# Kernel tuning notes

Hardware: AMD Instinct MI355X
Metric: run time of the kernel (lower is better)

Reference implementation:

```python
import jax, jax.numpy as jnp
import numpy as np

HID = 256        # constant.hidden_size
EMB = 256        # constant.embedding_size
STATE_NUM = 5    # constant.state_num
PAD_ID = 0


def _lstm(x, Wih, Whh, b):
    # x: (N, T, D) -> (N, T, H); single-layer unidirectional, PyTorch gate order i,f,g,o
    N = x.shape[0]
    Hh = Whh.shape[1]
    def step(carry, xt):
        h, c = carry
        g = xt @ Wih.T + h @ Whh.T + b
        i, f, gg, o = jnp.split(g, 4, axis=-1)
        c = jax.nn.sigmoid(f) * c + jax.nn.sigmoid(i) * jnp.tanh(gg)
        h = jax.nn.sigmoid(o) * jnp.tanh(c)
        return (h, c), h
    h0 = jnp.zeros((N, Hh), x.dtype)
    _, ys = jax.lax.scan(step, (h0, h0), jnp.swapaxes(x, 0, 1))
    return jnp.swapaxes(ys, 0, 1)


def setup_inputs() -> dict:
    rng = np.random.RandomState(0)
    B, L, W, V = 8, 128, 48, 50000
    S = STATE_NUM
    P = L // (S - 1)
    batch_utterances = jnp.asarray(rng.randint(0, V, size=(B, L, W)), jnp.int32)
    utterance_sequence_length = jnp.asarray(rng.randint(1, W + 1, size=(B, L)), jnp.int32)
    perm = np.stack([b * L + rng.permutation(L) for b in range(B)]).reshape(-1)
    session_transpose_matrix = jnp.asarray(perm, jnp.int32)
    stm = np.zeros((B, L, S), np.int32)  # col 0 == 0 -> new-state slot (projection path)
    carry = rng.rand(B, L, S - 1) < 0.3
    pos = rng.randint(1, P + 1, size=(B, L, S - 1))
    stm[:, :, 1:] = np.where(carry, -1, pos)
    state_transition_matrix = jnp.asarray(stm)

    def w(*shape):
        return jnp.asarray(rng.randn(*shape) * 0.05, jnp.float32)

    return dict(
        batch_utterances=batch_utterances,
        utterance_sequence_length=utterance_sequence_length,
        session_transpose_matrix=session_transpose_matrix,
        state_transition_matrix=state_transition_matrix,
        max_conversation_length=L,
        emb=w(V, EMB),
        utt_Wih=w(4 * HID, EMB), utt_Whh=w(4 * HID, HID), utt_b=w(4 * HID),
        ws1=w(HID, HID), ws2=w(1, HID),
        conv_Wih=w(4 * HID, HID), conv_Whh=w(4 * HID, HID), conv_b=w(4 * HID),
        sess_Wih=w(4 * HID, HID), sess_Whh=w(4 * HID, HID), sess_b=w(4 * HID),
        Wp=w(HID, 2 * HID), bp=w(HID),
        Ws=w(HID, 2 * HID), bs=w(HID),
    )


def reference(batch_utterances, utterance_sequence_length, session_transpose_matrix,
              state_transition_matrix, max_conversation_length,
              emb, utt_Wih, utt_Whh, utt_b, ws1, ws2,
              conv_Wih, conv_Whh, conv_b, sess_Wih, sess_Whh, sess_b,
              Wp, bp, Ws, bs):
    B, L, W = batch_utterances.shape
    S = STATE_NUM
    P = L // (S - 1)
    Lc = int(max_conversation_length)

    # --- UtteranceEncoder: embedding lookup + word-level LSTM ---
    tok = batch_utterances.reshape(-1, W)            # (B*L, W)
    word_out = _lstm(emb[tok], utt_Wih, utt_Whh, utt_b)  # (B*L, W, H)

    # --- SelfAttentiveEncoder (1 hop) ---
    hbar = jnp.tanh(word_out @ ws1.T)                # (B*L, W, H)
    logits = (hbar @ ws2.T)[..., 0]                  # (B*L, W)
    logits = logits + (-10000.0) * (tok == PAD_ID).astype(logits.dtype)
    alphas = jax.nn.softmax(logits, axis=1)
    att = jnp.einsum('nw,nwh->nh', alphas, word_out).reshape(B, L, HID)

    # --- ConversationEncoder ---
    conv = _lstm(att, conv_Wih, conv_Whh, conv_b)    # (B, L, H)

    # --- SessionEncoder: gather-permute utterances into sessions, LSTM per session ---
    flat = att.reshape(-1, HID)[session_transpose_matrix]       # (B*L, H)
    sess_in = flat.reshape(B * (S - 1), P, HID)
    sess_out = _lstm(sess_in, sess_Wih, sess_Whh, sess_b).reshape(B, S - 1, P, HID)

    # --- StateMatrixEncoder: sequential scatter/gather scan over conversation steps ---
    sess_idx = jnp.clip(jnp.arange(S) - 1, 0, S - 2)            # (S,)
    gathered = sess_out[:, sess_idx]                            # (B, S, P, H)
    conv_shift = jnp.concatenate([conv[:, :1], conv[:, :L - 1]], axis=1)  # conv_repre[i-1] (i==0 -> [0])
    stm_T = jnp.swapaxes(state_transition_matrix, 0, 1)         # (L, B, S)
    cs_T = jnp.swapaxes(conv_shift, 0, 1)                       # (L, B, H)

    def step(prev_row, inp):
        stm_i, cs = inp                                         # (B,S), (B,H)
        posn = jnp.clip(stm_i - 1, 0, P - 1)
        v_g = jnp.take_along_axis(gathered, posn[:, :, None, None], axis=2)[:, :, 0, :]  # (B,S,H)
        is_carry = (stm_i == -1)[..., None]
        is_gather = (stm_i > 0)[..., None]
        v = jnp.where(is_carry, prev_row, jnp.where(is_gather, v_g, 0.0))
        # AvgPool2d((S-1,1)) over exactly S-1 collected vectors == masked mean
        one_res = jnp.sum(jnp.where(stm_i[..., None] != 0, v, 0.0), axis=1) / (S - 1)
        new0 = jax.nn.relu(jnp.concatenate([one_res, cs], axis=-1) @ Wp.T + bp)
        row = jnp.where(is_gather, v_g, 0.0).at[:, 0, :].set(new0)
        return row, row

    _, rows = jax.lax.scan(step, jnp.zeros((B, S, HID), att.dtype), (stm_T, cs_T))
    state_matrix = jnp.swapaxes(rows, 0, 1)                     # (B, L, S, H)

    # --- ScoresCalculator (unidirectional -> LogSoftmax) ---
    uc = jnp.concatenate([att[:, :Lc], conv[:, :Lc]], axis=-1)  # (B, Lc, 2H)
    up = jax.nn.relu(uc @ Ws.T + bs)                            # (B, Lc, H)
    scores = jnp.einsum('blsh,blh->bls', state_matrix[:, :Lc], up)
    return jax.nn.log_softmax(scores, axis=2)
```

## Files before the change

### kernel.cpp

```cpp
#include <hip/hip_runtime.h>
#include <hip/hip_bf16.h>
#include <math.h>

#define HIDN 256
#define GATES 1024
#define BB 8
#define LLEN 128
#define WLEN 48
#define SNUM 5
#define PLEN 32
#define NSEQ 1024
#define EMBD 256

typedef _Float16 f16;
typedef _Float16 h2_t __attribute__((ext_vector_type(2)));
typedef short short8_t __attribute__((ext_vector_type(8)));
typedef float f32x4 __attribute__((ext_vector_type(4)));

__device__ __forceinline__ float sigf(float x){ return 1.0f/(1.0f+expf(-x)); }

__device__ __forceinline__ unsigned short f2bf(float f){
  unsigned int x = __builtin_bit_cast(unsigned int, f);
  x += 0x7fffu + ((x >> 16) & 1u);
  return (unsigned short)(x >> 16);
}
__device__ __forceinline__ float bf2f(unsigned short u){
  unsigned int x = ((unsigned int)u) << 16;
  return __builtin_bit_cast(float, x);
}

__device__ __forceinline__ float fd2(unsigned int w, unsigned int h, float acc){
  h2_t wa = __builtin_bit_cast(h2_t, w);
  h2_t hb = __builtin_bit_cast(h2_t, h);
#if defined(__has_builtin)
#if __has_builtin(__builtin_amdgcn_fdot2)
  return __builtin_amdgcn_fdot2(wa, hb, acc, false);
#else
  return acc + (float)wa[0]*(float)hb[0] + (float)wa[1]*(float)hb[1];
#endif
#else
  return acc + (float)wa[0]*(float)hb[0] + (float)wa[1]*(float)hb[1];
#endif
}

__device__ __forceinline__ float dot8(uint4 w, uint4 h, float acc){
  acc = fd2(w.x, h.x, acc);
  acc = fd2(w.y, h.y, acc);
  acc = fd2(w.z, h.z, acc);
  acc = fd2(w.w, h.w, acc);
  return acc;
}

template<bool GATHER, bool BIAS, bool RELU, bool SPLIT>
__global__ __launch_bounds__(256) void gemm_abt64_k(
  const float* __restrict__ A, const float* __restrict__ A2,
  const float* __restrict__ Bm, const float* __restrict__ bias,
  float* __restrict__ C, const int* __restrict__ gidx,
  int K, int N, int ostride)
{
  __shared__ float As[32][68];
  __shared__ float Bs[32][68];
  const int tid = threadIdx.x;
  const int m0 = blockIdx.x*64, n0 = blockIdx.y*64;
  const int tx = tid & 15, ty = tid >> 4;
  const int lr = tid >> 3;
  const int lc = (tid & 7) * 4;
  float acc[4][4] = {};
  for (int k0 = 0; k0 < K; k0 += 32){
    #pragma unroll
    for (int hf = 0; hf < 2; ++hf){
      const int r = lr + hf*32;
      int am = m0 + r;
      if (GATHER) am = gidx[am];
      const float* asrc;
      if (SPLIT){
        if (k0 < 256) asrc = A  + (size_t)am*256 + k0 + lc;
        else          asrc = A2 + (size_t)am*256 + (k0-256) + lc;
      } else {
        asrc = A + (size_t)am*K + k0 + lc;
      }
      float4 av = *reinterpret_cast<const float4*>(asrc);
      float4 bv = *reinterpret_cast<const float4*>(Bm + (size_t)(n0+r)*K + k0 + lc);
      As[lc+0][r]=av.x; As[lc+1][r]=av.y; As[lc+2][r]=av.z; As[lc+3][r]=av.w;
      Bs[lc+0][r]=bv.x; Bs[lc+1][r]=bv.y; Bs[lc+2][r]=bv.z; Bs[lc+3][r]=bv.w;
    }
    __syncthreads();
    #pragma unroll
    for (int kk = 0; kk < 32; ++kk){
      const float4 a = *reinterpret_cast<const float4*>(&As[kk][ty*4]);
      const float4 b = *reinterpret_cast<const float4*>(&Bs[kk][tx*4]);
      acc[0][0] += a.x*b.x; acc[0][1] += a.x*b.y; acc[0][2] += a.x*b.z; acc[0][3] += a.x*b.w;
      acc[1][0] += a.y*b.x; acc[1][1] += a.y*b.y; acc[1][2] += a.y*b.z; acc[1][3] += a.y*b.w;
      acc[2][0] += a.z*b.x; acc[2][1] += a.z*b.y; acc[2][2] += a.z*b.z; acc[2][3] += a.z*b.w;
      acc[3][0] += a.w*b.x; acc[3][1] += a.w*b.y; acc[3][2] += a.w*b.z; acc[3][3] += a.w*b.w;
    }
    __syncthreads();
  }
  float4 bb;
  if (BIAS) bb = *reinterpret_cast<const float4*>(bias + n0 + tx*4);
  else      { bb.x=0.f; bb.y=0.f; bb.z=0.f; bb.w=0.f; }
  #pragma unroll
  for (int i = 0; i < 4; ++i){
    float4 o;
    o.x = acc[i][0]+bb.x; o.y = acc[i][1]+bb.y; o.z = acc[i][2]+bb.z; o.w = acc[i][3]+bb.w;
    if (RELU){ o.x=fmaxf(o.x,0.f); o.y=fmaxf(o.y,0.f); o.z=fmaxf(o.z,0.f); o.w=fmaxf(o.w,0.f); }
    *reinterpret_cast<float4*>(C + (size_t)(m0+ty*4+i)*ostride + n0 + tx*4) = o;
  }
}

__global__ __launch_bounds__(256) void cvt_w16_k(
  const float* __restrict__ a, const float* __restrict__ b,
  f16* __restrict__ oa, f16* __restrict__ ob)
{
  const int i = blockIdx.x*256 + threadIdx.x;
  oa[i] = (f16)a[i];
  ob[i] = (f16)b[i];
}

__global__ __launch_bounds__(256) void cvt_bf16_k(
  const float* __restrict__ a, unsigned short* __restrict__ o, int n)
{
  for (int i = blockIdx.x*256 + threadIdx.x; i < n; i += gridDim.x*256)
    o[i] = f2bf(a[i]);
}

__global__ __launch_bounds__(256) void remap_k(const int* __restrict__ tok, int* __restrict__ gidx2){
  const int idx = blockIdx.x*256 + threadIdx.x;
  const int t = idx >> 10, u = idx & 1023;
  gidx2[idx] = tok[u*WLEN + t];
}

__global__ __launch_bounds__(256) void xgemm_k(
  const float* __restrict__ emb, const unsigned short* __restrict__ Wb,
  const float* __restrict__ bias, const int* __restrict__ gidx,
  float* __restrict__ X)
{
  __shared__ char As[32768];
  const int tid = threadIdx.x;
  const int w = tid >> 6, l = tid & 63;
  const int lr = l & 15, lg = l >> 4;
  const int m0 = blockIdx.x*64, n0 = blockIdx.y*64;
  #pragma unroll
  for (int rr = 0; rr < 4; ++rr){
    const int rl = rr*16 + (tid >> 4);
    const int c4 = tid & 15;
    const float* src = emb + (size_t)gidx[m0 + rl]*256;
    const int sw = (rl & 7) << 4;
    #pragma unroll
    for (int q = 0; q < 4; ++q){
      const int idx4 = c4 + q*16;
      float4 v = reinterpret_cast<const float4*>(src)[idx4];
      union { unsigned long long u; unsigned short us[4]; } pk;
      pk.us[0]=f2bf(v.x); pk.us[1]=f2bf(v.y); pk.us[2]=f2bf(v.z); pk.us[3]=f2bf(v.w);
      *reinterpret_cast<unsigned long long*>(As + rl*512 + ((idx4*8) ^ sw)) = pk.u;
    }
  }
  __syncthreads();
  short8_t a[8];
  #pragma unroll
  for (int ks = 0; ks < 8; ++ks){
    const int rl = w*16 + lr;
    a[ks] = *reinterpret_cast<const short8_t*>(As + rl*512 + ((ks*64 + lg*16) ^ ((rl&7)<<4)));
  }
  #pragma unroll
  for (int nt = 0; nt < 4; ++nt){
    f32x4 acc = f32x4{0,0,0,0};
    const int n = n0 + nt*16 + lr;
    #pragma unroll
    for (int ks = 0; ks < 8; ++ks){
      short8_t b = *reinterpret_cast<const short8_t*>(Wb + (size_t)n*256 + ks*32 + lg*8);
      acc = __builtin_amdgcn_mfma_f32_16x16x32_bf16(a[ks], b, acc, 0, 0, 0);
    }
    const float bn = bias[n];
    #pragma unroll
    for (int r = 0; r < 4; ++r){
      const int m = m0 + w*16 + lg*4 + r;
      X[(size_t)m*1024 + n] = acc[r] + bn;
    }
  }
}

__global__ __launch_bounds__(256, 1) void word_stream_k(
  const float* __restrict__ X, const unsigned short* __restrict__ Wb,
  unsigned short* __restrict__ woutb)
{
  extern __shared__ char smem[];
  const int tid = threadIdx.x;
  const int w = tid >> 6, l = tid & 63;
  const int lr = l & 15, lg = l >> 4;
  const int S0 = blockIdx.x * 16;
  char* wlds = smem + w*32768;
  char* hb0 = smem + 131072;
  char* hb1 = smem + 139264;

  #pragma unroll
  for (int rr = 0; rr < 16; ++rr){
    const int rl = rr*4 + lg;
    const unsigned short* src = Wb + (size_t)(768 + w*64 + rl)*256;
    const int sw = (rl & 7) << 4;
    short8_t v0 = *reinterpret_cast<const short8_t*>(src + lr*8);
    short8_t v1 = *reinterpret_cast<const short8_t*>(src + (lr+16)*8);
    *reinterpret_cast<short8_t*>(wlds + rl*512 + ((lr*16) ^ sw)) = v0;
    *reinterpret_cast<short8_t*>(wlds + rl*512 + (((lr+16)*16) ^ sw)) = v1;
  }
  short8_t wr[96];
  #pragma unroll
  for (int g = 0; g < 3; ++g){
    #pragma unroll
    for (int jt = 0; jt < 4; ++jt){
      #pragma unroll
      for (int ks = 0; ks < 8; ++ks){
        const int n = g*256 + w*64 + jt*16 + lr;
        wr[(g*4 + jt)*8 + ks] = *reinterpret_cast<const short8_t*>(
            Wb + (size_t)n*256 + ks*32 + lg*8);
      }
    }
  }
  float c_reg[4][4] = {};
  __syncthreads();

  for (int t = 0; t < WLEN; ++t){
    const char* hr = (t & 1) ? hb1 : hb0;
    char* hw = (t & 1) ? hb0 : hb1;
    #pragma unroll
    for (int jt = 0; jt < 4; ++jt){
      f32x4 acc0 = f32x4{0,0,0,0}, acc1 = f32x4{0,0,0,0};
      f32x4 acc2 = f32x4{0,0,0,0}, acc3 = f32x4{0,0,0,0};
      #pragma unroll
      for (int ks = 0; ks < 8; ++ks){
        short8_t a;
        if (t == 0){
          a = short8_t{0,0,0,0,0,0,0,0};
        } else {
          const int kb = ks*64 + lg*16;
          a = *reinterpret_cast<const short8_t*>(hr + lr*512 + (kb ^ ((lr & 7) << 4)));
        }
        acc0 = __builtin_amdgcn_mfma_f32_16x16x32_bf16(a, wr[(0*4+jt)*8+ks], acc0, 0, 0, 0);
        acc1 = __builtin_amdgcn_mfma_f32_16x16x32_bf16(a, wr[(1*4+jt)*8+ks], acc1, 0, 0, 0);
        acc2 = __builtin_amdgcn_mfma_f32_16x16x32_bf16(a, wr[(2*4+jt)*8+ks], acc2, 0, 0, 0);
        const int rl_o = jt*16 + lr;
        short8_t bo = *reinterpret_cast<const short8_t*>(
            wlds + rl_o*512 + ((ks*64 + lg*16) ^ ((rl_o & 7) << 4)));
        acc3 = __builtin_amdgcn_mfma_f32_16x16x32_bf16(a, bo, acc3, 0, 0, 0);
      }
      const int j = w*64 + jt*16 + lr;
      #pragma unroll
      for (int r = 0; r < 4; ++r){
        const int s = lg*4 + r;
        const float* xp = X + ((size_t)t*1024 + (S0+s))*1024 + j;
        float gi = acc0[r] + xp[0];
        float gf = acc1[r] + xp[256];
        float gg = acc2[r] + xp[512];
        float go = acc3[r] + xp[768];
        float cc = sigf(gf)*c_reg[jt][r] + sigf(gi)*tanhf(gg);
        c_reg[jt][r] = cc;
        float hh = sigf(go)*tanhf(cc);
        unsigned short hb16 = f2bf(hh);
        woutb[((size_t)(S0+s)*WLEN + t)*256 + j] = hb16;
        *reinterpret_cast<unsigned short*>(hw + s*512 + ((j*2) ^ ((s & 7) << 4))) = hb16;
      }
    }
    __syncthreads();
  }
}

__global__ __launch_bounds__(256) void attlog_k(
  const unsigned short* __restrict__ woutb, const unsigned short* __restrict__ ws1b,
  const float* __restrict__ ws2, float* __restrict__ logits)
{
  const int tid = threadIdx.x;
  const int w = tid >> 6, l = tid & 63;
  const int lr = l & 15, lg = l >> 4;
  const int m0 = blockIdx.x*64;
  short8_t a[8];
  #pragma unroll
  for (int ks = 0; ks < 8; ++ks){
    const int m = m0 + w*16 + lr;
    a[ks] = *reinterpret_cast<const short8_t*>(woutb + (size_t)m*256 + ks*32 + lg*8);
  }
  float part[4] = {0.f, 0.f, 0.f, 0.f};
  #pragma unroll
  for (int nt = 0; nt < 16; ++nt){
    f32x4 acc = f32x4{0,0,0,0};
    const int n = nt*16 + lr;
    #pragma unroll
    for (int ks = 0; ks < 8; ++ks){
      short8_t b = *reinterpret_cast<const short8_t*>(ws1b + (size_t)n*256 + ks*32 + lg*8);
      acc = __builtin_amdgcn_mfma_f32_16x16x32_bf16(a[ks], b, acc, 0, 0, 0);
    }
    const float w2 = ws2[n];
    #pragma unroll
    for (int r = 0; r < 4; ++r) part[r] += w2 * tanhf(acc[r]);
  }
  #pragma unroll
  for (int r = 0; r < 4; ++r){
    float p = part[r];
    p += __shfl_xor(p, 1, 64);
    p += __shfl_xor(p, 2, 64);
    p += __shfl_xor(p, 4, 64);
    p += __shfl_xor(p, 8, 64);
    if (lr == 0) logits[m0 + w*16 + lg*4 + r] = p;
  }
}

__global__ __launch_bounds__(256) void att_softmax_k(
  const unsigned short* __restrict__ woutb, const float* __restrict__ logits,
  const int* __restrict__ tok, float* __restrict__ att)
{
  __shared__ float e[WLEN];
  __shared__ float den_s;
  const int n = blockIdx.x, j = threadIdx.x;
  if (j < WLEN){
    float lgt = logits[n*WLEN + j];
    if (tok[n*WLEN + j] == 0) lgt -= 10000.0f;
    e[j] = lgt;
  }
  __syncthreads();
  if (j == 0){
    float mx = -1e30f;
    for (int ww = 0; ww < WLEN; ++ww) mx = fmaxf(mx, e[ww]);
    float den = 0.f;
    for (int ww = 0; ww < WLEN; ++ww){ float ee = expf(e[ww]-mx); e[ww] = ee; den += ee; }
    den_s = den;
  }
  __syncthreads();
  const float inv = 1.0f/den_s;
  float a = 0.f;
  for (int ww = 0; ww < WLEN; ++ww)
    a += e[ww]*bf2f(woutb[((size_t)n*WLEN + ww)*HIDN + j]);
  att[(size_t)n*HIDN + j] = a*inv;
}

__global__ __launch_bounds__(256) void word_gates_k(
    const int* __restrict__ tok, const float* __restrict__ emb,
    const float* __restrict__ Wih, const float* __restrict__ Whh,
    const float* __restrict__ bias, const float* __restrict__ hbuf,
    float* __restrict__ G, int t)
{
  __shared__ float As[32][68];
  __shared__ float Bs[32][68];
  const int tid = threadIdx.x;
  const int m0 = blockIdx.x*64, n0 = blockIdx.y*64;
  const int tx = tid & 15, ty = tid >> 4;
  const int lr = tid >> 3;
  const int lc = (tid & 7) * 4;
  float acc[4][4] = {};
  for (int kt = 0; kt < 16; ++kt){
    const int k0 = (kt & 7)*32;
    const bool xp = (kt < 8);
    #pragma unroll
    for (int hf = 0; hf < 2; ++hf){
      const int r = lr + hf*32;
      float4 av, bv;
      if (xp){
        const int token = tok[(m0+r)*WLEN + t];
        av = *reinterpret_cast<const float4*>(emb + (size_t)token*EMBD + k0 + lc);
      } else {
        av = *reinterpret_cast<const float4*>(hbuf + (size_t)(m0+r)*HIDN + k0 + lc);
      }
      const float* bptr = (xp ? Wih : Whh) + (size_t)(n0+r)*HIDN + k0 + lc;
      bv = *reinterpret_cast<const float4*>(bptr);
      As[lc+0][r]=av.x; As[lc+1][r]=av.y; As[lc+2][r]=av.z; As[lc+3][r]=av.w;
      Bs[lc+0][r]=bv.x; Bs[lc+1][r]=bv.y; Bs[lc+2][r]=bv.z; Bs[lc+3][r]=bv.w;
    }
    __syncthreads();
    #pragma unroll
    for (int kk = 0; kk < 32; ++kk){
      const float4 a = *reinterpret_cast<const float4*>(&As[kk][ty*4]);
      const float4 b = *reinterpret_cast<const float4*>(&Bs[kk][tx*4]);
      acc[0][0] += a.x*b.x; acc[0][1] += a.x*b.y; acc[0][2] += a.x*b.z; acc[0][3] += a.x*b.w;
      acc[1][0] += a.y*b.x; acc[1][1] += a.y*b.y; acc[1][2] += a.y*b.z; acc[1][3] += a.y*b.w;
      acc[2][0] += a.z*b.x; acc[2][1] += a.z*b.y; acc[2][2] += a.z*b.z; acc[2][3] += a.z*b.w;
      acc[3][0] += a.w*b.x; acc[3][1] += a.w*b.y; acc[3][2] += a.w*b.z; acc[3][3] += a.w*b.w;
    }
    __syncthreads();
  }
  const float4 bb = *reinterpret_cast<const float4*>(bias + n0 + tx*4);
  #pragma unroll
  for (int i = 0; i < 4; ++i){
    float4 o;
    o.x = acc[i][0]+bb.x; o.y = acc[i][1]+bb.y; o.z = acc[i][2]+bb.z; o.w = acc[i][3]+bb.w;
    *reinterpret_cast<float4*>(G + (size_t)(m0+ty*4+i)*GATES + n0 + tx*4) = o;
  }
}

__global__ __launch_bounds__(256) void word_update_k(
  const float* __restrict__ G, float* __restrict__ h, float* __restrict__ c,
  unsigned short* __restrict__ woutb, int t)
{
  int idx = blockIdx.x*256 + threadIdx.x;
  int m = idx >> 8, j = idx & 255;
  const float* g = G + (size_t)m*GATES;
  float gi = g[j], gf = g[HIDN+j], gg = g[2*HIDN+j], go = g[3*HIDN+j];
  float cc = c[idx];
  cc = sigf(gf)*cc + sigf(gi)*tanhf(gg);
  float hh = sigf(go)*tanhf(cc);
  c[idx] = cc; h[idx] = hh;
  woutb[(size_t)m*WLEN*HIDN + (size_t)t*HIDN + j] = f2bf(hh);
}

__global__ __launch_bounds__(512, 2) void recur512_k(
  const float* __restrict__ xwc, const f16* __restrict__ w16c, float* __restrict__ convb,
  const float* __restrict__ xws, const f16* __restrict__ w16s, float* __restrict__ soutb)
{
  const float* xw; const f16* w16; float* out; int seq, T;
  if (blockIdx.x < 8){ seq = blockIdx.x;     T = 128; xw = xwc; w16 = w16c; out = convb; }
  else               { seq = blockIdx.x - 8; T = 32;  xw = xws; w16 = w16s; out = soutb; }

  extern __shared__ char smem[];
  uint4* w_lds  = (uint4*)smem;
  float* g_s    = (float*)(smem + 131072);
  f16*   h_half = (f16*)(smem + 131072 + 4096);
  const uint4* h4 = (const uint4*)h_half;

  const int tid = threadIdx.x;
  const int n0 = tid, n1 = tid + 512;

  #pragma unroll
  for (int cth = 0; cth < 8; ++cth){
    w_lds[cth*1024 + n0] = *reinterpret_cast<const uint4*>(w16 + (size_t)n0*HIDN + 192 + cth*8);
    w_lds[cth*1024 + n1] = *reinterpret_cast<const uint4*>(w16 + (size_t)n1*HIDN + 192 + cth*8);
  }
  uint4 wr0[24], wr1[24];
  #pragma unroll
  for (int cth = 0; cth < 24; ++cth){
    wr0[cth] = *reinterpret_cast<const uint4*>(w16 + (size_t)n0*HIDN + cth*8);
    wr1[cth] = *reinterpret_cast<const uint4*>(w16 + (size_t)n1*HIDN + cth*8);
  }
  if (tid < 128) reinterpret_cast<uint4*>(h_half)[tid >> 2] = uint4{0,0,0,0};
  float c_reg = 0.f;
  __syncthreads();

  for (int t = 0; t < T; ++t){
    float acc0 = xw[(size_t)(seq*T + t)*GATES + n0];
    float acc1 = xw[(size_t)(seq*T + t)*GATES + n1];
    float a0=0.f, a1=0.f, a2=0.f, a3=0.f;
    #pragma unroll
    for (int k = 0; k < 24; k += 4){
      const uint4 h0 = h4[k+0], h1 = h4[k+1], h2 = h4[k+2], h3 = h4[k+3];
      a0 = dot8(wr0[k+0], h0, a0);
      a1 = dot8(wr0[k+1], h1, a1);
      a2 = dot8(wr0[k+2], h2, a2);
      a3 = dot8(wr0[k+3], h3, a3);
      acc1 = dot8(wr1[k+0], h0, acc1);
      acc1 = dot8(wr1[k+1], h1, acc1);
      acc1 = dot8(wr1[k+2], h2, acc1);
      acc1 = dot8(wr1[k+3], h3, acc1);
    }
    #pragma unroll
    for (int cth = 0; cth < 8; ++cth){
      const uint4 hv = h4[24 + cth];
      const uint4 w0 = w_lds[cth*1024 + n0];
      const uint4 w1 = w_lds[cth*1024 + n1];
      a0 = dot8(w0, hv, a0);
      acc1 = dot8(w1, hv, acc1);
    }
    g_s[n0] = acc0 + (a0+a1) + (a2+a3);
    g_s[n1] = acc1;
    __syncthreads();
    if (tid < HIDN){
      const int j = tid;
      float gi = g_s[j], gf = g_s[HIDN+j], gg = g_s[2*HIDN+j], go = g_s[3*HIDN+j];
      float cc = sigf(gf)*c_reg + sigf(gi)*tanhf(gg);
      c_reg = cc;
      float hh = sigf(go)*tanhf(cc);
      h_half[j] = (f16)hh;
      out[(size_t)(seq*T + t)*HIDN + j] = hh;
    }
    __syncthreads();
  }
}

__global__ __launch_bounds__(256) void scan_prep_k(
  const float* __restrict__ sess_out, const float* __restrict__ conv_out,
  const int* __restrict__ stm, float* __restrict__ state, float* __restrict__ onec)
{
  const int bl = blockIdx.x;
  const int b = bl >> 7, l = bl & 127;
  const int j = threadIdx.x;
  float ones = 0.f;
  #pragma unroll
  for (int s = 1; s < SNUM; ++s){
    const int sv = stm[(size_t)bl*SNUM + s];
    float vg = 0.f;
    if (sv > 0){
      int p = sv - 1; if (p > PLEN-1) p = PLEN-1;
      vg = sess_out[((size_t)(b*4 + (s-1))*PLEN + p)*HIDN + j];
    }
    float v = vg;
    if (sv == -1){
      v = 0.f;
      if (l > 0){
        const int pv = stm[(size_t)(bl-1)*SNUM + s];
        if (pv > 0){
          int p2 = pv - 1; if (p2 > PLEN-1) p2 = PLEN-1;
          v = sess_out[((size_t)(b*4 + (s-1))*PLEN + p2)*HIDN + j];
        }
      }
    }
    if (sv != 0) ones += v;
    state[((size_t)bl*SNUM + s)*HIDN + j] = vg;
  }
  onec[(size_t)bl*(2*HIDN) + j] = ones * 0.25f;
  const int lp = (l == 0) ? 0 : (l-1);
  onec[(size_t)bl*(2*HIDN) + HIDN + j] = conv_out[((size_t)(b*LLEN + lp))*HIDN + j];
}

__global__ __launch_bounds__(256) void scores_k(
  const float* __restrict__ state, const float* __restrict__ up, float* __restrict__ out)
{
  const int n = blockIdx.x, j = threadIdx.x;
  __shared__ float red[SNUM][4];
  const float u = up[(size_t)n*HIDN + j];
  const int lane = j & 63, wid = j >> 6;
  #pragma unroll
  for (int s = 0; s < SNUM; ++s){
    float p = state[((size_t)n*SNUM + s)*HIDN + j]*u;
    for (int off = 32; off; off >>= 1) p += __shfl_down(p, off, 64);
    if (lane == 0) red[s][wid] = p;
  }
  __syncthreads();
  if (j == 0){
    float sc[SNUM]; float mx = -1e30f;
    #pragma unroll
    for (int s = 0; s < SNUM; ++s){
      sc[s] = red[s][0]+red[s][1]+red[s][2]+red[s][3];
      mx = fmaxf(mx, sc[s]);
    }
    float den = 0.f;
    #pragma unroll
    for (int s = 0; s < SNUM; ++s) den += expf(sc[s]-mx);
    const float ls = logf(den);
    #pragma unroll
    for (int s = 0; s < SNUM; ++s) out[(size_t)n*SNUM + s] = sc[s]-mx-ls;
  }
}

static const size_t OFF_G     = 0;
static const size_t OFF_H     = OFF_G     + 1048576;
static const size_t OFF_C     = OFF_H     + 262144;
static const size_t OFF_ATT   = OFF_C     + 262144;
static const size_t OFF_XWC   = OFF_ATT   + 262144;
static const size_t OFF_XWS   = OFF_XWC   + 1048576;
static const size_t OFF_CONV  = OFF_XWS   + 1048576;
static const size_t OFF_SOUT  = OFF_CONV  + 262144;
static const size_t OFF_STATE = OFF_SOUT  + 262144;
static const size_t OFF_ONEC  = OFF_STATE + 1310720;
static const size_t OFF_UP    = OFF_ONEC  + 524288;
static const size_t OFF_LOG   = OFF_UP    + 262144;
static const size_t OFF_GIDX2 = OFF_LOG   + 49152;
static const size_t OFF_W16C  = OFF_GIDX2 + 49152;
static const size_t OFF_W16S  = OFF_W16C  + 131072;
static const size_t OFF_UWHHB = OFF_W16S  + 131072;
static const size_t OFF_WIHB  = OFF_UWHHB + 131072;
static const size_t OFF_WS1B  = OFF_WIHB  + 131072;
static const size_t OFF_WOUTB = OFF_WS1B  + 32768;
static const size_t OFF_X     = OFF_WOUTB + 6291456;
static const size_t NEED_X_FLOATS = OFF_X + (size_t)49152*1024;

static const size_t WORD_LDS_BYTES  = 131072 + 2*8192;
static const size_t RECUR_LDS_BYTES = 131072 + 4096 + 512;

extern "C" void kernel_launch(void* const* d_in, const int* in_sizes, int n_in,
                              void* d_out, int out_size, void* d_ws, size_t ws_size,
                              hipStream_t stream)
{
  const int*   tok   = (const int*)  d_in[0];
  const int*   perm  = (const int*)  d_in[2];
  const int*   stm   = (const int*)  d_in[3];
  const float* emb   = (const float*)d_in[5];
  const float* uWih  = (const float*)d_in[6];
  const float* uWhh  = (const float*)d_in[7];
  const float* ub    = (const float*)d_in[8];
  const float* ws1   = (const float*)d_in[9];
  const float* ws2   = (const float*)d_in[10];
  const float* cWih  = (const float*)d_in[11];
  const float* cWhh  = (const float*)d_in[12];
  const float* cb    = (const float*)d_in[13];
  const float* sWih  = (const float*)d_in[14];
  const float* sWhh  = (const float*)d_in[15];
  const float* sb    = (const float*)d_in[16];
  const float* Wp    = (const float*)d_in[17];
  const float* bp    = (const float*)d_in[18];
  const float* Ws    = (const float*)d_in[19];
  const float* bs    = (const float*)d_in[20];

  float* wsf    = (float*)d_ws;
  float* G      = wsf + OFF_G;
  float* h      = wsf + OFF_H;
  float* c      = wsf + OFF_C;
  float* att    = wsf + OFF_ATT;
  float* xwc    = wsf + OFF_XWC;
  float* xws    = wsf + OFF_XWS;
  float* convb  = wsf + OFF_CONV;
  float* soutb  = wsf + OFF_SOUT;
  float* statem = wsf + OFF_STATE;
  float* onec   = wsf + OFF_ONEC;
  float* upb    = wsf + OFF_UP;
  float* logits = wsf + OFF_LOG;
  int*   gidx2  = (int*)(wsf + OFF_GIDX2);
  f16*   w16c   = (f16*)(wsf + OFF_W16C);
  f16*   w16s   = (f16*)(wsf + OFF_W16S);
  unsigned short* uwhhb = (unsigned short*)(wsf + OFF_UWHHB);
  unsigned short* wihb  = (unsigned short*)(wsf + OFF_WIHB);
  unsigned short* ws1b  = (unsigned short*)(wsf + OFF_WS1B);
  unsigned short* woutb = (unsigned short*)(wsf + OFF_WOUTB);
  float* X      = wsf + OFF_X;

  const bool useX = ws_size >= NEED_X_FLOATS*sizeof(float);

  hipFuncSetAttribute(reinterpret_cast<const void*>(word_stream_k),
                      hipFuncAttributeMaxDynamicSharedMemorySize, (int)WORD_LDS_BYTES);
  hipFuncSetAttribute(reinterpret_cast<const void*>(recur512_k),
                      hipFuncAttributeMaxDynamicSharedMemorySize, (int)RECUR_LDS_BYTES);

  cvt_w16_k<<<1024, 256, 0, stream>>>(cWhh, sWhh, w16c, w16s);
  cvt_bf16_k<<<256, 256, 0, stream>>>(uWhh, uwhhb, 262144);
  cvt_bf16_k<<<256, 256, 0, stream>>>(uWih, wihb, 262144);
  cvt_bf16_k<<<64, 256, 0, stream>>>(ws1, ws1b, 65536);

  if (useX){
    remap_k<<<192, 256, 0, stream>>>(tok, gidx2);
    xgemm_k<<<dim3(768,16), 256, 0, stream>>>(emb, wihb, ub, gidx2, X);
    word_stream_k<<<64, 256, WORD_LDS_BYTES, stream>>>(X, uwhhb, woutb);
  } else {
    hipMemsetAsync(h, 0, 2*262144*sizeof(float), stream);
    for (int t = 0; t < WLEN; ++t){
      word_gates_k<<<dim3(16,16), 256, 0, stream>>>(tok, emb, uWih, uWhh, ub, h, G, t);
      word_update_k<<<1024, 256, 0, stream>>>(G, h, c, woutb, t);
    }
  }

  attlog_k<<<768, 256, 0, stream>>>(woutb, ws1b, ws2, logits);
  att_softmax_k<<<1024, 256, 0, stream>>>(woutb, logits, tok, att);

  gemm_abt64_k<false,true,false,false><<<dim3(16,16), 256, 0, stream>>>(
    att, nullptr, cWih, cb, xwc, nullptr, 256, GATES, GATES);
  gemm_abt64_k<true,true,false,false><<<dim3(16,16), 256, 0, stream>>>(
    att, nullptr, sWih, sb, xws, perm, 256, GATES, GATES);

  recur512_k<<<40, 512, RECUR_LDS_BYTES, stream>>>(xwc, w16c, convb, xws, w16s, soutb);

  scan_prep_k<<<1024, 256, 0, stream>>>(soutb, convb, stm, statem, onec);
  gemm_abt64_k<false,true,true,false><<<dim3(16,4), 256, 0, stream>>>(
    onec, nullptr, Wp, bp, statem, nullptr, 512, HIDN, SNUM*HIDN);

  gemm_abt64_k<false,true,true,true><<<dim3(16,4), 256, 0, stream>>>(
    att, convb, Ws, bs, upb, nullptr, 512, HIDN, HIDN);
  scores_k<<<1024, 256, 0, stream>>>(statem, upb, (float*)d_out);
}
```

Baseline: 1.257 ms.

## Store word input gates as interleaved bf16 and use MFMA for conv/session projections

The word-level input projection now writes bf16 instead of fp32, with the four gates interleaved per hidden unit. The recurrent kernel therefore reads one 8-byte load per unit and moves half the X traffic. The word recurrence no longer holds most Whh weights in registers; it streams the i/f/g tiles from global memory (L2) each step and keeps only the o tile in LDS. It also zero-initialises h in LDS instead of branching on t==0. The conv and session input GEMMs now use a generic bf16 MFMA kernel on a bf16 copy of att. The conv/session recurrence runs 1024 threads with one gate row per thread. The trade-off is bf16 rounding of the gate pre-activations and per-step weight reloads from cache.

After: 1.668 ms. 32.7% more time.

```diff
diff --git a/kernel.cpp b/kernel.cpp
--- a/kernel.cpp
+++ b/kernel.cpp
@@ -4,12 +4,10 @@
 
 #define HIDN 256
 #define GATES 1024
-#define BB 8
 #define LLEN 128
 #define WLEN 48
 #define SNUM 5
 #define PLEN 32
-#define NSEQ 1024
 #define EMBD 256
 
 typedef _Float16 f16;
@@ -42,7 +40,6 @@
   return acc + (float)wa[0]*(float)hb[0] + (float)wa[1]*(float)hb[1];
 #endif
 }
-
 __device__ __forceinline__ float dot8(uint4 w, uint4 h, float acc){
   acc = fd2(w.x, h.x, acc);
   acc = fd2(w.y, h.y, acc);
@@ -108,6 +105,21 @@
   }
 }
 
+__global__ __launch_bounds__(256) void cvt2_k(
+  const float* __restrict__ a, const float* __restrict__ b,
+  unsigned short* __restrict__ oa, unsigned short* __restrict__ ob, int n)
+{
+  for (int i = blockIdx.x*256 + threadIdx.x; i < n; i += gridDim.x*256){
+    oa[i] = f2bf(a[i]);
+    ob[i] = f2bf(b[i]);
+  }
+}
+__global__ __launch_bounds__(256) void cvt1_k(
+  const float* __restrict__ a, unsigned short* __restrict__ o, int n)
+{
+  for (int i = blockIdx.x*256 + threadIdx.x; i < n; i += gridDim.x*256)
+    o[i] = f2bf(a[i]);
+}
 __global__ __launch_bounds__(256) void cvt_w16_k(
   const float* __restrict__ a, const float* __restrict__ b,
   f16* __restrict__ oa, f16* __restrict__ ob)
@@ -115,13 +127,6 @@
   const int i = blockIdx.x*256 + threadIdx.x;
   oa[i] = (f16)a[i];
   ob[i] = (f16)b[i];
-}
-
-__global__ __launch_bounds__(256) void cvt_bf16_k(
-  const float* __restrict__ a, unsigned short* __restrict__ o, int n)
-{
-  for (int i = blockIdx.x*256 + threadIdx.x; i < n; i += gridDim.x*256)
-    o[i] = f2bf(a[i]);
 }
 
 __global__ __launch_bounds__(256) void remap_k(const int* __restrict__ tok, int* __restrict__ gidx2){
@@ -130,10 +135,11 @@
   gidx2[idx] = tok[u*WLEN + t];
 }
 
-__global__ __launch_bounds__(256) void xgemm_k(
-  const float* __restrict__ emb, const unsigned short* __restrict__ Wb,
+template<int AMODE, bool OUT16, bool XPERM>
+__global__ __launch_bounds__(256) void mmabt_k(
+  const void* __restrict__ Asrc, const unsigned short* __restrict__ Wb,
   const float* __restrict__ bias, const int* __restrict__ gidx,
-  float* __restrict__ X)
+  void* __restrict__ Cout)
 {
   __shared__ char As[32768];
   const int tid = threadIdx.x;
@@ -141,18 +147,23 @@
   const int lr = l & 15, lg = l >> 4;
   const int m0 = blockIdx.x*64, n0 = blockIdx.y*64;
   #pragma unroll
-  for (int rr = 0; rr < 4; ++rr){
-    const int rl = rr*16 + (tid >> 4);
-    const int c4 = tid & 15;
-    const float* src = emb + (size_t)gidx[m0 + rl]*256;
-    const int sw = (rl & 7) << 4;
-    #pragma unroll
-    for (int q = 0; q < 4; ++q){
-      const int idx4 = c4 + q*16;
-      float4 v = reinterpret_cast<const float4*>(src)[idx4];
-      union { unsigned long long u; unsigned short us[4]; } pk;
-      pk.us[0]=f2bf(v.x); pk.us[1]=f2bf(v.y); pk.us[2]=f2bf(v.z); pk.us[3]=f2bf(v.w);
-      *reinterpret_cast<unsigned long long*>(As + rl*512 + ((idx4*8) ^ sw)) = pk.u;
+  for (int q = 0; q < 8; ++q){
+    const int ck = tid*8 + q;
+    const int rl = ck >> 5, o16 = ck & 31;
+    int row = m0 + rl;
+    if (AMODE <= 1) row = gidx[row];
+    char* dst = As + rl*512 + ((o16*16) ^ ((rl & 7) << 4));
+    if (AMODE == 0){
+      const float* src = (const float*)Asrc + (size_t)row*256 + o16*8;
+      float4 f0 = *reinterpret_cast<const float4*>(src);
+      float4 f1 = *reinterpret_cast<const float4*>(src + 4);
+      union { short8_t s; unsigned short u[8]; } pk;
+      pk.u[0]=f2bf(f0.x); pk.u[1]=f2bf(f0.y); pk.u[2]=f2bf(f0.z); pk.u[3]=f2bf(f0.w);
+      pk.u[4]=f2bf(f1.x); pk.u[5]=f2bf(f1.y); pk.u[6]=f2bf(f1.z); pk.u[7]=f2bf(f1.w);
+      *reinterpret_cast<short8_t*>(dst) = pk.s;
+    } else {
+      *reinterpret_cast<short8_t*>(dst) = *reinterpret_cast<const short8_t*>(
+          (const unsigned short*)Asrc + (size_t)row*256 + o16*8);
     }
   }
   __syncthreads();
@@ -160,7 +171,7 @@
   #pragma unroll
   for (int ks = 0; ks < 8; ++ks){
     const int rl = w*16 + lr;
-    a[ks] = *reinterpret_cast<const short8_t*>(As + rl*512 + ((ks*64 + lg*16) ^ ((rl&7)<<4)));
+    a[ks] = *reinterpret_cast<const short8_t*>(As + rl*512 + ((ks*64 + lg*16) ^ ((rl & 7) << 4)));
   }
   #pragma unroll
   for (int nt = 0; nt < 4; ++nt){
@@ -172,16 +183,19 @@
       acc = __builtin_amdgcn_mfma_f32_16x16x32_bf16(a[ks], b, acc, 0, 0, 0);
     }
     const float bn = bias[n];
+    const int nn = XPERM ? ((n & 255)*4 + (n >> 8)) : n;
     #pragma unroll
     for (int r = 0; r < 4; ++r){
       const int m = m0 + w*16 + lg*4 + r;
-      X[(size_t)m*1024 + n] = acc[r] + bn;
-    }
-  }
-}
-
-__global__ __launch_bounds__(256, 1) void word_stream_k(
-  const float* __restrict__ X, const unsigned short* __restrict__ Wb,
+      if (OUT16) ((unsigned short*)Cout)[(size_t)m*1024 + nn] = f2bf(acc[r] + bn);
+      else       ((float*)Cout)[(size_t)m*1024 + nn] = acc[r] + bn;
+    }
+  }
+}
+
+__global__ __launch_bounds__(256, 1) void word3_k(
+  const unsigned short* __restrict__ Xp,
+  const unsigned short* __restrict__ Wb,
   unsigned short* __restrict__ woutb)
 {
   extern __shared__ char smem[];
@@ -190,75 +204,139 @@
   const int lr = l & 15, lg = l >> 4;
   const int S0 = blockIdx.x * 16;
   char* wlds = smem + w*32768;
-  char* hb0 = smem + 131072;
-  char* hb1 = smem + 139264;
-
-  #pragma unroll
-  for (int rr = 0; rr < 16; ++rr){
-    const int rl = rr*4 + lg;
-    const unsigned short* src = Wb + (size_t)(768 + w*64 + rl)*256;
-    const int sw = (rl & 7) << 4;
-    short8_t v0 = *reinterpret_cast<const short8_t*>(src + lr*8);
-    short8_t v1 = *reinterpret_cast<const short8_t*>(src + (lr+16)*8);
-    *reinterpret_cast<short8_t*>(wlds + rl*512 + ((lr*16) ^ sw)) = v0;
-    *reinterpret_cast<short8_t*>(wlds + rl*512 + (((lr+16)*16) ^ sw)) = v1;
-  }
-  short8_t wr[96];
-  #pragma unroll
-  for (int g = 0; g < 3; ++g){
-    #pragma unroll
-    for (int jt = 0; jt < 4; ++jt){
-      #pragma unroll
-      for (int ks = 0; ks < 8; ++ks){
-        const int n = g*256 + w*64 + jt*16 + lr;
-        wr[(g*4 + jt)*8 + ks] = *reinterpret_cast<const short8_t*>(
-            Wb + (size_t)n*256 + ks*32 + lg*8);
-      }
-    }
-  }
+  char* hb0  = smem + 131072;
+  char* hb1  = smem + 139264;
+
+  #pragma unroll
+  for (int q = 0; q < 4; ++q)
+    reinterpret_cast<uint4*>(smem + 131072)[q*256 + tid] = uint4{0,0,0,0};
+
+  #pragma unroll
+  for (int q = 0; q < 32; ++q){
+    const int ck = l*32 + q;
+    const int rl = ck >> 5, o16 = ck & 31;
+    short8_t v = *reinterpret_cast<const short8_t*>(
+        Wb + (size_t)(768 + w*64 + rl)*256 + o16*8);
+    *reinterpret_cast<short8_t*>(wlds + rl*512 + ((o16*16) ^ ((rl & 7) << 4))) = v;
+  }
+  short8_t wi[2][8];
+  #pragma unroll
+  for (int jt = 0; jt < 2; ++jt)
+    #pragma unroll
+    for (int ks = 0; ks < 8; ++ks)
+      wi[jt][ks] = *reinterpret_cast<const short8_t*>(
+          Wb + (size_t)(w*64 + jt*16 + lr)*256 + ks*32 + lg*8);
+
+  const unsigned short* ib = Wb + (size_t)(      32 + w*64 + lr)*256 + lg*8;
+  const unsigned short* fb = Wb + (size_t)(256      + w*64 + lr)*256 + lg*8;
+  const unsigned short* gb = Wb + (size_t)(512      + w*64 + lr)*256 + lg*8;
   float c_reg[4][4] = {};
   __syncthreads();
 
   for (int t = 0; t < WLEN; ++t){
     const char* hr = (t & 1) ? hb1 : hb0;
     char* hw = (t & 1) ? hb0 : hb1;
+    const unsigned short* pi = ib;
+    const unsigned short* pf = fb;
+    const unsigned short* pg = gb;
+    asm volatile("" : "+v"(pi), "+v"(pf), "+v"(pg));
+    short8_t a[8];
+    #pragma unroll
+    for (int ks = 0; ks < 8; ++ks)
+      a[ks] = *reinterpret_cast<const short8_t*>(
+          hr + lr*512 + ((ks*64 + lg*16) ^ ((lr & 7) << 4)));
     #pragma unroll
     for (int jt = 0; jt < 4; ++jt){
-      f32x4 acc0 = f32x4{0,0,0,0}, acc1 = f32x4{0,0,0,0};
-      f32x4 acc2 = f32x4{0,0,0,0}, acc3 = f32x4{0,0,0,0};
+      f32x4 aI = f32x4{0,0,0,0}, aF = f32x4{0,0,0,0};
+      f32x4 aG = f32x4{0,0,0,0}, aO = f32x4{0,0,0,0};
       #pragma unroll
       for (int ks = 0; ks < 8; ++ks){
-        short8_t a;
-        if (t == 0){
-          a = short8_t{0,0,0,0,0,0,0,0};
-        } else {
-          const int kb = ks*64 + lg*16;
-          a = *reinterpret_cast<const short8_t*>(hr + lr*512 + (kb ^ ((lr & 7) << 4)));
-        }
-        acc0 = __builtin_amdgcn_mfma_f32_16x16x32_bf16(a, wr[(0*4+jt)*8+ks], acc0, 0, 0, 0);
-        acc1 = __builtin_amdgcn_mfma_f32_16x16x32_bf16(a, wr[(1*4+jt)*8+ks], acc1, 0, 0, 0);
-        acc2 = __builtin_amdgcn_mfma_f32_16x16x32_bf16(a, wr[(2*4+jt)*8+ks], acc2, 0, 0, 0);
+        short8_t bi;
+        if (jt < 2) bi = wi[jt][ks];
+        else        bi = *reinterpret_cast<const short8_t*>(pi + (size_t)((jt-2)*16)*256 + ks*32);
+        short8_t bf = *reinterpret_cast<const short8_t*>(pf + (size_t)(jt*16)*256 + ks*32);
+        short8_t bg = *reinterpret_cast<const short8_t*>(pg + (size_t)(jt*16)*256 + ks*32);
         const int rl_o = jt*16 + lr;
         short8_t bo = *reinterpret_cast<const short8_t*>(
             wlds + rl_o*512 + ((ks*64 + lg*16) ^ ((rl_o & 7) << 4)));
-        acc3 = __builtin_amdgcn_mfma_f32_16x16x32_bf16(a, bo, acc3, 0, 0, 0);
+        aI = __builtin_amdgcn_mfma_f32_16x16x32_bf16(a[ks], bi, aI, 0, 0, 0);
+        aF = __builtin_amdgcn_mfma_f32_16x16x32_bf16(a[ks], bf, aF, 0, 0, 0);
+        aG = __builtin_amdgcn_mfma_f32_16x16x32_bf16(a[ks], bg, aG, 0, 0, 0);
+        aO = __builtin_amdgcn_mfma_f32_16x16x32_bf16(a[ks], bo, aO, 0, 0, 0);
       }
       const int j = w*64 + jt*16 + lr;
       #pragma unroll
       for (int r = 0; r < 4; ++r){
         const int s = lg*4 + r;
-        const float* xp = X + ((size_t)t*1024 + (S0+s))*1024 + j;
-        float gi = acc0[r] + xp[0];
-        float gf = acc1[r] + xp[256];
-        float gg = acc2[r] + xp[512];
-        float go = acc3[r] + xp[768];
+        unsigned long long xv = *reinterpret_cast<const unsigned long long*>(
+            Xp + ((size_t)t*1024 + (S0+s))*1024 + j*4);
+        float gi = aI[r] + bf2f((unsigned short)(xv));
+        float gf = aF[r] + bf2f((unsigned short)(xv >> 16));
+        float gg = aG[r] + bf2f((unsigned short)(xv >> 32));
+        float go = aO[r] + bf2f((unsigned short)(xv >> 48));
         float cc = sigf(gf)*c_reg[jt][r] + sigf(gi)*tanhf(gg);
         c_reg[jt][r] = cc;
         float hh = sigf(go)*tanhf(cc);
-        unsigned short hb16 = f2bf(hh);
-        woutb[((size_t)(S0+s)*WLEN + t)*256 + j] = hb16;
-        *reinterpret_cast<unsigned short*>(hw + s*512 + ((j*2) ^ ((s & 7) << 4))) = hb16;
+        unsigned short h16 = f2bf(hh);
+        woutb[((size_t)(S0+s)*WLEN + t)*256 + j] = h16;
+        *reinterpret_cast<unsigned short*>(hw + s*512 + ((j*2) ^ ((s & 7) << 4))) = h16;
       }
+    }
+    __syncthreads();
+  }
+}
+
+__global__ __launch_bounds__(1024) void recur3_k(
+  const float* __restrict__ xwc, const f16* __restrict__ w16c, float* __restrict__ convb,
+  const float* __restrict__ xws, const f16* __restrict__ w16s, float* __restrict__ soutb)
+{
+  const float* xw; const f16* w16; float* out; int seq, T;
+  if (blockIdx.x < 8){ seq = blockIdx.x;     T = 128; xw = xwc; w16 = w16c; out = convb; }
+  else               { seq = blockIdx.x - 8; T = 32;  xw = xws; w16 = w16s; out = soutb; }
+
+  extern __shared__ char smem[];
+  uint4* w_lds  = (uint4*)smem;
+  float* g_s    = (float*)(smem + 131072);
+  f16*   h_half = (f16*)(smem + 131072 + 4096);
+  const uint4* h4 = (const uint4*)h_half;
+
+  const int tid = threadIdx.x;
+  #pragma unroll
+  for (int cth = 0; cth < 8; ++cth)
+    w_lds[cth*1024 + tid] = *reinterpret_cast<const uint4*>(w16 + (size_t)tid*256 + 192 + cth*8);
+  uint4 wr[24];
+  #pragma unroll
+  for (int cth = 0; cth < 24; ++cth)
+    wr[cth] = *reinterpret_cast<const uint4*>(w16 + (size_t)tid*256 + cth*8);
+  if (tid < 32) reinterpret_cast<uint4*>(h_half)[tid] = uint4{0,0,0,0};
+  float c_reg = 0.f;
+  __syncthreads();
+
+  for (int t = 0; t < T; ++t){
+    float acc = xw[(size_t)(seq*T + t)*GATES + tid];
+    float a0 = 0.f, a1 = 0.f;
+    #pragma unroll
+    for (int k = 0; k < 24; k += 2){
+      const uint4 h0 = h4[k], h1 = h4[k+1];
+      a0 = dot8(wr[k],   h0, a0);
+      a1 = dot8(wr[k+1], h1, a1);
+    }
+    #pragma unroll
+    for (int cth = 0; cth < 8; cth += 2){
+      const uint4 h0 = h4[24+cth], h1 = h4[25+cth];
+      a0 = dot8(w_lds[cth*1024 + tid],     h0, a0);
+      a1 = dot8(w_lds[(cth+1)*1024 + tid], h1, a1);
+    }
+    g_s[tid] = acc + a0 + a1;
+    __syncthreads();
+    if (tid < HIDN){
+      const int j = tid;
+      float gi = g_s[j], gf = g_s[HIDN+j], gg = g_s[2*HIDN+j], go = g_s[3*HIDN+j];
+      float cc = sigf(gf)*c_reg + sigf(gi)*tanhf(gg);
+      c_reg = cc;
+      float hh = sigf(go)*tanhf(cc);
+      h_half[j] = (f16)hh;
+      out[(size_t)(seq*T + t)*HIDN + j] = hh;
     }
     __syncthreads();
   }
@@ -305,7 +383,7 @@
 
 __global__ __launch_bounds__(256) void att_softmax_k(
   const unsigned short* __restrict__ woutb, const float* __restrict__ logits,
-  const int* __restrict__ tok, float* __restrict__ att)
+  const int* __restrict__ tok, float* __restrict__ att, unsigned short* __restrict__ attb)
 {
   __shared__ float e[WLEN];
   __shared__ float den_s;
@@ -328,7 +406,9 @@
   float a = 0.f;
   for (int ww = 0; ww < WLEN; ++ww)
     a += e[ww]*bf2f(woutb[((size_t)n*WLEN + ww)*HIDN + j]);
-  att[(size_t)n*HIDN + j] = a*inv;
+  a *= inv;
+  att[(size_t)n*HIDN + j] = a;
+  attb[(size_t)n*HIDN + j] = f2bf(a);
 }
 
 __global__ __launch_bounds__(256) void word_gates_k(
@@ -399,78 +479,6 @@
   woutb[(size_t)m*WLEN*HIDN + (size_t)t*HIDN + j] = f2bf(hh);
 }
 
-__global__ __launch_bounds__(512, 2) void recur512_k(
-  const float* __restrict__ xwc, const f16* __restrict__ w16c, float* __restrict__ convb,
-  const float* __restrict__ xws, const f16* __restrict__ w16s, float* __restrict__ soutb)
-{
-  const float* xw; const f16* w16; float* out; int seq, T;
-  if (blockIdx.x < 8){ seq = blockIdx.x;     T = 128; xw = xwc; w16 = w16c; out = convb; }
-  else               { seq = blockIdx.x - 8; T = 32;  xw = xws; w16 = w16s; out = soutb; }
-
-  extern __shared__ char smem[];
-  uint4* w_lds  = (uint4*)smem;
-  float* g_s    = (float*)(smem + 131072);
-  f16*   h_half = (f16*)(smem + 131072 + 4096);
-  const uint4* h4 = (const uint4*)h_half;
-
-  const int tid = threadIdx.x;
-  const int n0 = tid, n1 = tid + 512;
-
-  #pragma unroll
-  for (int cth = 0; cth < 8; ++cth){
-    w_lds[cth*1024 + n0] = *reinterpret_cast<const uint4*>(w16 + (size_t)n0*HIDN + 192 + cth*8);
-    w_lds[cth*1024 + n1] = *reinterpret_cast<const uint4*>(w16 + (size_t)n1*HIDN + 192 + cth*8);
-  }
-  uint4 wr0[24], wr1[24];
-  #pragma unroll
-  for (int cth = 0; cth < 24; ++cth){
-    wr0[cth] = *reinterpret_cast<const uint4*>(w16 + (size_t)n0*HIDN + cth*8);
-    wr1[cth] = *reinterpret_cast<const uint4*>(w16 + (size_t)n1*HIDN + cth*8);
-  }
-  if (tid < 128) reinterpret_cast<uint4*>(h_half)[tid >> 2] = uint4{0,0,0,0};
-  float c_reg = 0.f;
-  __syncthreads();
-
-  for (int t = 0; t < T; ++t){
-    float acc0 = xw[(size_t)(seq*T + t)*GATES + n0];
-    float acc1 = xw[(size_t)(seq*T + t)*GATES + n1];
-    float a0=0.f, a1=0.f, a2=0.f, a3=0.f;
-    #pragma unroll
-    for (int k = 0; k < 24; k += 4){
-      const uint4 h0 = h4[k+0], h1 = h4[k+1], h2 = h4[k+2], h3 = h4[k+3];
-      a0 = dot8(wr0[k+0], h0, a0);
-      a1 = dot8(wr0[k+1], h1, a1);
-      a2 = dot8(wr0[k+2], h2, a2);
-      a3 = dot8(wr0[k+3], h3, a3);
-      acc1 = dot8(wr1[k+0], h0, acc1);
-      acc1 = dot8(wr1[k+1], h1, acc1);
-      acc1 = dot8(wr1[k+2], h2, acc1);
-      acc1 = dot8(wr1[k+3], h3, acc1);
-    }
-    #pragma unroll
-    for (int cth = 0; cth < 8; ++cth){
-      const uint4 hv = h4[24 + cth];
-      const uint4 w0 = w_lds[cth*1024 + n0];
-      const uint4 w1 = w_lds[cth*1024 + n1];
-      a0 = dot8(w0, hv, a0);
-      acc1 = dot8(w1, hv, acc1);
-    }
-    g_s[n0] = acc0 + (a0+a1) + (a2+a3);
-    g_s[n1] = acc1;
-    __syncthreads();
-    if (tid < HIDN){
-      const int j = tid;
-      float gi = g_s[j], gf = g_s[HIDN+j], gg = g_s[2*HIDN+j], go = g_s[3*HIDN+j];
-      float cc = sigf(gf)*c_reg + sigf(gi)*tanhf(gg);
-      c_reg = cc;
-      float hh = sigf(go)*tanhf(cc);
-      h_half[j] = (f16)hh;
-      out[(size_t)(seq*T + t)*HIDN + j] = hh;
-    }
-    __syncthreads();
-  }
-}
-
 __global__ __launch_bounds__(256) void scan_prep_k(
   const float* __restrict__ sess_out, const float* __restrict__ conv_out,
   const int* __restrict__ stm, float* __restrict__ state, float* __restrict__ onec)
@@ -540,7 +548,8 @@
 static const size_t OFF_H     = OFF_G     + 1048576;
 static const size_t OFF_C     = OFF_H     + 262144;
 static const size_t OFF_ATT   = OFF_C     + 262144;
-static const size_t OFF_XWC   = OFF_ATT   + 262144;
+static const size_t OFF_ATTB  = OFF_ATT   + 262144;
+static const size_t OFF_XWC   = OFF_ATTB  + 131072;
 static const size_t OFF_XWS   = OFF_XWC   + 1048576;
 static const size_t OFF_CONV  = OFF_XWS   + 1048576;
 static const size_t OFF_SOUT  = OFF_CONV  + 262144;
@@ -549,16 +558,18 @@
 static const size_t OFF_UP    = OFF_ONEC  + 524288;
 static const size_t OFF_LOG   = OFF_UP    + 262144;
 static const size_t OFF_GIDX2 = OFF_LOG   + 49152;
-static const size_t OFF_W16C  = OFF_GIDX2 + 49152;
-static const size_t OFF_W16S  = OFF_W16C  + 131072;
-static const size_t OFF_UWHHB = OFF_W16S  + 131072;
+static const size_t OFF_UWHHB = OFF_GIDX2 + 49152;
 static const size_t OFF_WIHB  = OFF_UWHHB + 131072;
 static const size_t OFF_WS1B  = OFF_WIHB  + 131072;
-static const size_t OFF_WOUTB = OFF_WS1B  + 32768;
+static const size_t OFF_CWIHB = OFF_WS1B  + 32768;
+static const size_t OFF_SWIHB = OFF_CWIHB + 131072;
+static const size_t OFF_W16C  = OFF_SWIHB + 131072;
+static const size_t OFF_W16S  = OFF_W16C  + 131072;
+static const size_t OFF_WOUTB = OFF_W16S  + 131072;
 static const size_t OFF_X     = OFF_WOUTB + 6291456;
-static const size_t NEED_X_FLOATS = OFF_X + (size_t)49152*1024;
-
-static const size_t WORD_LDS_BYTES  = 131072 + 2*8192;
+static const size_t NEED_X_FLOATS = OFF_X + (size_t)49152*512;
+
+static const size_t WORD_LDS_BYTES  = 131072 + 16384;
 static const size_t RECUR_LDS_BYTES = 131072 + 4096 + 512;
 
 extern "C" void kernel_launch(void* const* d_in, const int* in_sizes, int n_in,
@@ -599,30 +610,33 @@
   float* upb    = wsf + OFF_UP;
   float* logits = wsf + OFF_LOG;
   int*   gidx2  = (int*)(wsf + OFF_GIDX2);
-  f16*   w16c   = (f16*)(wsf + OFF_W16C);
-  f16*   w16s   = (f16*)(wsf + OFF_W16S);
+  unsigned short* attb  = (unsigned short*)(wsf + OFF_ATTB);
   unsigned short* uwhhb = (unsigned short*)(wsf + OFF_UWHHB);
   unsigned short* wihb  = (unsigned short*)(wsf + OFF_WIHB);
   unsigned short* ws1b  = (unsigned short*)(wsf + OFF_WS1B);
+  unsigned short* cwihb = (unsigned short*)(wsf + OFF_CWIHB);
+  unsigned short* swihb = (unsigned short*)(wsf + OFF_SWIHB);
+  f16*   w16c   = (f16*)(wsf + OFF_W16C);
+  f16*   w16s   = (f16*)(wsf + OFF_W16S);
   unsigned short* woutb = (unsigned short*)(wsf + OFF_WOUTB);
-  float* X      = wsf + OFF_X;
+  unsigned short* X16   = (unsigned short*)(wsf + OFF_X);
 
   const bool useX = ws_size >= NEED_X_FLOATS*sizeof(float);
 
-  hipFuncSetAttribute(reinterpret_cast<const void*>(word_stream_k),
+  hipFuncSetAttribute(reinterpret_cast<const void*>(word3_k),
                       hipFuncAttributeMaxDynamicSharedMemorySize, (int)WORD_LDS_BYTES);
-  hipFuncSetAttribute(reinterpret_cast<const void*>(recur512_k),
+  hipFuncSetAttribute(reinterpret_cast<const void*>(recur3_k),
                       hipFuncAttributeMaxDynamicSharedMemorySize, (int)RECUR_LDS_BYTES);
 
+  cvt2_k<<<256, 256, 0, stream>>>(uWhh, uWih, uwhhb, wihb, 262144);
+  cvt2_k<<<256, 256, 0, stream>>>(cWih, sWih, cwihb, swihb, 262144);
   cvt_w16_k<<<1024, 256, 0, stream>>>(cWhh, sWhh, w16c, w16s);
-  cvt_bf16_k<<<256, 256, 0, stream>>>(uWhh, uwhhb, 262144);
-  cvt_bf16_k<<<256, 256, 0, stream>>>(uWih, wihb, 262144);
-  cvt_bf16_k<<<64, 256, 0, stream>>>(ws1, ws1b, 65536);
+  cvt1_k<<<64, 256, 0, stream>>>(ws1, ws1b, 65536);
 
   if (useX){
     remap_k<<<192, 256, 0, stream>>>(tok, gidx2);
-    xgemm_k<<<dim3(768,16), 256, 0, stream>>>(emb, wihb, ub, gidx2, X);
-    word_stream_k<<<64, 256, WORD_LDS_BYTES, stream>>>(X, uwhhb, woutb);
+    mmabt_k<0,true,true><<<dim3(768,16), 256, 0, stream>>>(emb, wihb, ub, gidx2, X16);
+    word3_k<<<64, 256, WORD_LDS_BYTES, stream>>>(X16, uwhhb, woutb);
   } else {
     hipMemsetAsync(h, 0, 2*262144*sizeof(float), stream);
     for (int t = 0; t < WLEN; ++t){
@@ -632,14 +646,12 @@
   }
 
   attlog_k<<<768, 256, 0, stream>>>(woutb, ws1b, ws2, logits);
-  att_softmax_k<<<1024, 256, 0, stream>>>(woutb, logits, tok, att);
-
-  gemm_abt64_k<false,true,false,false><<<dim3(16,16), 256, 0, stream>>>(
-    att, nullptr, cWih, cb, xwc, nullptr, 256, GATES, GATES);
-  gemm_abt64_k<true,true,false,false><<<dim3(16,16), 256, 0, stream>>>(
-    att, nullptr, sWih, sb, xws, perm, 256, GATES, GATES);
-
-  recur512_k<<<40, 512, RECUR_LDS_BYTES, stream>>>(xwc, w16c, convb, xws, w16s, soutb);
+  att_softmax_k<<<1024, 256, 0, stream>>>(woutb, logits, tok, att, attb);
+
+  mmabt_k<2,false,false><<<dim3(16,16), 256, 0, stream>>>(attb, cwihb, cb, nullptr, xwc);
+  mmabt_k<1,false,false><<<dim3(16,16), 256, 0, stream>>>(attb, swihb, sb, perm, xws);
+
+  recur3_k<<<40, 1024, RECUR_LDS_BYTES, stream>>>(xwc, w16c, convb, xws, w16s, soutb);
 
   scan_prep_k<<<1024, 256, 0, stream>>>(soutb, convb, stm, statem, onec);
   gemm_abt64_k<false,true,true,false><<<dim3(16,4), 256, 0, stream>>>(
```
